# Optimization experiments

Hardware: AMD Instinct MI355X
Metric: run time of the kernel (lower is better)

Reference implementation:

```python
import jax, jax.numpy as jnp
import numpy as np

B, N, C = 8, 4096, 768
H = 12
D = C // H            # 64
BN = C // 2           # bottleneck dim 384
EPS_LN = 1e-5
EPS_ATTN = 1e-6


def layer_norm(x, g, b):
    mu = jnp.mean(x, axis=-1, keepdims=True)
    var = jnp.mean(jnp.square(x - mu), axis=-1, keepdims=True)
    return (x - mu) * jax.lax.rsqrt(var + EPS_LN) * g + b


def setup_inputs() -> dict:
    key = jax.random.key(0)
    ks = jax.random.split(key, 8)
    s = 0.02
    return {
        "x": jax.random.normal(ks[0], (B, N, C), jnp.float32),
        "w_qkv": jax.random.normal(ks[1], (C, 3 * C), jnp.float32) * s,
        "b_qkv": jnp.zeros((3 * C,), jnp.float32),
        "w_proj": jax.random.normal(ks[2], (C, C), jnp.float32) * s,
        "b_proj": jnp.zeros((C,), jnp.float32),
        "g1": jnp.ones((C,), jnp.float32),
        "beta1": jnp.zeros((C,), jnp.float32),
        "g2": jnp.ones((C,), jnp.float32),
        "beta2": jnp.zeros((C,), jnp.float32),
        "w_down": jax.random.normal(ks[3], (C, BN), jnp.float32) * s,
        "b_down": jnp.zeros((BN,), jnp.float32),
        "w_up": jax.random.normal(ks[4], (BN, C), jnp.float32) * s,
        "b_up": jnp.zeros((C,), jnp.float32),
        "g3": jnp.ones((C,), jnp.float32),
        "beta3": jnp.zeros((C,), jnp.float32),
    }


def _linear_attention(x, w_qkv, b_qkv, w_proj, b_proj):
    # x: (B, N, C)
    qkv = x @ w_qkv + b_qkv                       # (B, N, 3C)
    qkv = qkv.reshape(B, N, 3, H, D)
    qkv = jnp.transpose(qkv, (2, 0, 3, 1, 4))     # (3, B, H, N, D)
    q, k, v = qkv[0], qkv[1], qkv[2]
    fm = lambda t: jax.nn.elu(t) + 1.0            # positive feature map
    q, k = fm(q), fm(k)
    kv = jnp.einsum('bhnd,bhnv->bhdv', k, v)      # (B, H, D, D)
    out = jnp.einsum('bhnd,bhdv->bhnv', q, kv)    # (B, H, N, D)
    k_sum = k.sum(axis=2)                         # (B, H, D)
    normalizer = jnp.einsum('bhnd,bhd->bhn', q, k_sum) + EPS_ATTN
    out = out / normalizer[..., None]
    out = jnp.transpose(out, (0, 2, 1, 3)).reshape(B, N, C)
    return out @ w_proj + b_proj


def reference(x, w_qkv, b_qkv, w_proj, b_proj, g1, beta1, g2, beta2,
              w_down, b_down, w_up, b_up, g3, beta3):
    # DinomalyBlock forward (eval mode: dropout/noise disabled)
    x = x + _linear_attention(layer_norm(x, g1, beta1), w_qkv, b_qkv, w_proj, b_proj)
    r = layer_norm(x, g2, beta2)
    h = jax.nn.gelu(r @ w_down + b_down, approximate=False)  # torch GELU default = exact
    h = h @ w_up + b_up
    return layer_norm(r + h, g3, beta3)
```

## Files before the change

kernel.cpp:

```cpp
#include <hip/hip_runtime.h>
#include <hip/hip_bf16.h>
#include <cstdio>


typedef __attribute__((ext_vector_type(8))) short short8;
typedef __attribute__((ext_vector_type(4))) float floatx4;

__device__ __forceinline__ float bf2f(unsigned short u) {
    return __uint_as_float(((unsigned int)u) << 16);
}
__device__ __forceinline__ unsigned short f2bf(float f) {
    __hip_bfloat16 h = __float2bfloat16(f);
    return *reinterpret_cast<unsigned short*>(&h);
}

__device__ __forceinline__ void async_copy16(const unsigned short* g, unsigned short* l) {
    __builtin_amdgcn_global_load_lds(
        (const __attribute__((address_space(1))) unsigned int*)g,
        (__attribute__((address_space(3))) unsigned int*)l, 16, 0, 0);
}

__device__ __forceinline__ floatx4 MFMA16(short8 a, short8 b, floatx4 c) {
    return __builtin_amdgcn_mfma_f32_16x16x32_bf16(a, b, c, 0, 0, 0);
}

__global__ __launch_bounds__(256) void transpose_all(
    const float* __restrict__ wq, const float* __restrict__ wp,
    const float* __restrict__ wd, const float* __restrict__ wu,
    unsigned short* __restrict__ tq, unsigned short* __restrict__ tp,
    unsigned short* __restrict__ td, unsigned short* __restrict__ tu)
{
    int blk = blockIdx.x;
    const float* w; unsigned short* o; int K, Nc, tx32;
    if (blk < 1728)      { w = wq; o = tq; K = 768; Nc = 2304; tx32 = 24; }
    else if (blk < 2304) { w = wp; o = tp; K = 768; Nc = 768;  tx32 = 24; blk -= 1728; }
    else if (blk < 2592) { w = wd; o = td; K = 768; Nc = 384;  tx32 = 24; blk -= 2304; }
    else                 { w = wu; o = tu; K = 384; Nc = 768;  tx32 = 12; blk -= 2592; }
    int kb = (blk % tx32) * 32, nb = (blk / tx32) * 32;
    __shared__ float tile[32][33];
    int tx = threadIdx.x & 31, ty = threadIdx.x >> 5;
    #pragma unroll
    for (int i = 0; i < 32; i += 8)
        tile[ty + i][tx] = w[(size_t)(kb + ty + i) * Nc + nb + tx];
    __syncthreads();
    #pragma unroll
    for (int i = 0; i < 32; i += 8)
        o[(size_t)(nb + ty + i) * K + kb + tx] = f2bf(tile[tx][ty + i]);
}

template<bool OBF16>
__global__ __launch_bounds__(256) void ln_kernel(
    const float* __restrict__ in, const float* __restrict__ gw,
    const float* __restrict__ bw, void* __restrict__ outp)
{
    int t = threadIdx.x;
    int lane = t & 63, wave = t >> 6;
    int row = blockIdx.x * 4 + wave;
    const float4* src = (const float4*)(in + (size_t)row * 768);
    float4 x0 = src[lane], x1 = src[lane + 64], x2 = src[lane + 128];
    float s  = (x0.x + x0.y + x0.z + x0.w)
             + (x1.x + x1.y + x1.z + x1.w)
             + (x2.x + x2.y + x2.z + x2.w);
    float ss = (x0.x * x0.x + x0.y * x0.y + x0.z * x0.z + x0.w * x0.w)
             + (x1.x * x1.x + x1.y * x1.y + x1.z * x1.z + x1.w * x1.w)
             + (x2.x * x2.x + x2.y * x2.y + x2.z * x2.z + x2.w * x2.w);
    #pragma unroll
    for (int o = 1; o < 64; o <<= 1) {
        s += __shfl_xor(s, o);
        ss += __shfl_xor(ss, o);
    }
    float mu = s * (1.0f / 768.0f);
    float var = ss * (1.0f / 768.0f) - mu * mu;
    float rstd = rsqrtf(var + 1e-5f);
    float4 g0 = ((const float4*)gw)[lane], g1 = ((const float4*)gw)[lane + 64],
           g2 = ((const float4*)gw)[lane + 128];
    float4 b0 = ((const float4*)bw)[lane], b1 = ((const float4*)bw)[lane + 64],
           b2 = ((const float4*)bw)[lane + 128];
    float4 y0, y1, y2;
    y0.x = (x0.x - mu) * rstd * g0.x + b0.x; y0.y = (x0.y - mu) * rstd * g0.y + b0.y;
    y0.z = (x0.z - mu) * rstd * g0.z + b0.z; y0.w = (x0.w - mu) * rstd * g0.w + b0.w;
    y1.x = (x1.x - mu) * rstd * g1.x + b1.x; y1.y = (x1.y - mu) * rstd * g1.y + b1.y;
    y1.z = (x1.z - mu) * rstd * g1.z + b1.z; y1.w = (x1.w - mu) * rstd * g1.w + b1.w;
    y2.x = (x2.x - mu) * rstd * g2.x + b2.x; y2.y = (x2.y - mu) * rstd * g2.y + b2.y;
    y2.z = (x2.z - mu) * rstd * g2.z + b2.z; y2.w = (x2.w - mu) * rstd * g2.w + b2.w;
    if (OBF16) {
        uint2* dst = (uint2*)outp + (size_t)row * 192;
        uint2 p0, p1, p2;
        p0.x = (unsigned int)f2bf(y0.x) | ((unsigned int)f2bf(y0.y) << 16);
        p0.y = (unsigned int)f2bf(y0.z) | ((unsigned int)f2bf(y0.w) << 16);
        p1.x = (unsigned int)f2bf(y1.x) | ((unsigned int)f2bf(y1.y) << 16);
        p1.y = (unsigned int)f2bf(y1.z) | ((unsigned int)f2bf(y1.w) << 16);
        p2.x = (unsigned int)f2bf(y2.x) | ((unsigned int)f2bf(y2.y) << 16);
        p2.y = (unsigned int)f2bf(y2.z) | ((unsigned int)f2bf(y2.w) << 16);
        dst[lane] = p0; dst[lane + 64] = p1; dst[lane + 128] = p2;
    } else {
        float4* dst = (float4*)outp + (size_t)row * 192;
        dst[lane] = y0; dst[lane + 64] = y1; dst[lane + 128] = y2;
    }
}

template<bool RES_F32, bool OUT_F32>
__global__ __launch_bounds__(256) void add_ln_kernel(
    const unsigned short* __restrict__ y, const void* __restrict__ resv,
    const float* __restrict__ gw, const float* __restrict__ bw,
    void* __restrict__ outp)
{
    int t = threadIdx.x;
    int lane = t & 63, wave = t >> 6;
    int row = blockIdx.x * 4 + wave;
    const uint2* ysrc = (const uint2*)(y + (size_t)row * 768);
    uint2 ya = ysrc[lane], yb = ysrc[lane + 64], yc = ysrc[lane + 128];
    float v[12];
    v[0] = bf2f((unsigned short)(ya.x & 0xffff)); v[1] = bf2f((unsigned short)(ya.x >> 16));
    v[2] = bf2f((unsigned short)(ya.y & 0xffff)); v[3] = bf2f((unsigned short)(ya.y >> 16));
    v[4] = bf2f((unsigned short)(yb.x & 0xffff)); v[5] = bf2f((unsigned short)(yb.x >> 16));
    v[6] = bf2f((unsigned short)(yb.y & 0xffff)); v[7] = bf2f((unsigned short)(yb.y >> 16));
    v[8] = bf2f((unsigned short)(yc.x & 0xffff)); v[9] = bf2f((unsigned short)(yc.x >> 16));
    v[10] = bf2f((unsigned short)(yc.y & 0xffff)); v[11] = bf2f((unsigned short)(yc.y >> 16));
    if (RES_F32) {
        const float4* rsrc = (const float4*)((const float*)resv + (size_t)row * 768);
        float4 r0 = rsrc[lane], r1 = rsrc[lane + 64], r2 = rsrc[lane + 128];
        v[0] += r0.x; v[1] += r0.y; v[2] += r0.z; v[3] += r0.w;
        v[4] += r1.x; v[5] += r1.y; v[6] += r1.z; v[7] += r1.w;
        v[8] += r2.x; v[9] += r2.y; v[10] += r2.z; v[11] += r2.w;
    } else {
        const uint2* rsrc = (const uint2*)((const unsigned short*)resv + (size_t)row * 768);
        uint2 r0 = rsrc[lane], r1 = rsrc[lane + 64], r2 = rsrc[lane + 128];
        v[0] += bf2f((unsigned short)(r0.x & 0xffff)); v[1] += bf2f((unsigned short)(r0.x >> 16));
        v[2] += bf2f((unsigned short)(r0.y & 0xffff)); v[3] += bf2f((unsigned short)(r0.y >> 16));
        v[4] += bf2f((unsigned short)(r1.x & 0xffff)); v[5] += bf2f((unsigned short)(r1.x >> 16));
        v[6] += bf2f((unsigned short)(r1.y & 0xffff)); v[7] += bf2f((unsigned short)(r1.y >> 16));
        v[8] += bf2f((unsigned short)(r2.x & 0xffff)); v[9] += bf2f((unsigned short)(r2.x >> 16));
        v[10] += bf2f((unsigned short)(r2.y & 0xffff)); v[11] += bf2f((unsigned short)(r2.y >> 16));
    }
    float s = 0.f, ss = 0.f;
    #pragma unroll
    for (int i = 0; i < 12; i++) { s += v[i]; ss += v[i] * v[i]; }
    #pragma unroll
    for (int o = 1; o < 64; o <<= 1) {
        s += __shfl_xor(s, o);
        ss += __shfl_xor(ss, o);
    }
    float mu = s * (1.0f / 768.0f);
    float var = ss * (1.0f / 768.0f) - mu * mu;
    float rstd = rsqrtf(var + 1e-5f);
    float4 g0 = ((const float4*)gw)[lane], g1 = ((const float4*)gw)[lane + 64],
           g2 = ((const float4*)gw)[lane + 128];
    float4 b0 = ((const float4*)bw)[lane], b1 = ((const float4*)bw)[lane + 64],
           b2 = ((const float4*)bw)[lane + 128];
    float yv[12];
    yv[0] = (v[0] - mu) * rstd * g0.x + b0.x; yv[1] = (v[1] - mu) * rstd * g0.y + b0.y;
    yv[2] = (v[2] - mu) * rstd * g0.z + b0.z; yv[3] = (v[3] - mu) * rstd * g0.w + b0.w;
    yv[4] = (v[4] - mu) * rstd * g1.x + b1.x; yv[5] = (v[5] - mu) * rstd * g1.y + b1.y;
    yv[6] = (v[6] - mu) * rstd * g1.z + b1.z; yv[7] = (v[7] - mu) * rstd * g1.w + b1.w;
    yv[8] = (v[8] - mu) * rstd * g2.x + b2.x; yv[9] = (v[9] - mu) * rstd * g2.y + b2.y;
    yv[10] = (v[10] - mu) * rstd * g2.z + b2.z; yv[11] = (v[11] - mu) * rstd * g2.w + b2.w;
    if (OUT_F32) {
        float4* dst = (float4*)outp + (size_t)row * 192;
        dst[lane] = make_float4(yv[0], yv[1], yv[2], yv[3]);
        dst[lane + 64] = make_float4(yv[4], yv[5], yv[6], yv[7]);
        dst[lane + 128] = make_float4(yv[8], yv[9], yv[10], yv[11]);
    } else {
        uint2* dst = (uint2*)outp + (size_t)row * 192;
        uint2 p0, p1, p2;
        p0.x = (unsigned int)f2bf(yv[0]) | ((unsigned int)f2bf(yv[1]) << 16);
        p0.y = (unsigned int)f2bf(yv[2]) | ((unsigned int)f2bf(yv[3]) << 16);
        p1.x = (unsigned int)f2bf(yv[4]) | ((unsigned int)f2bf(yv[5]) << 16);
        p1.y = (unsigned int)f2bf(yv[6]) | ((unsigned int)f2bf(yv[7]) << 16);
        p2.x = (unsigned int)f2bf(yv[8]) | ((unsigned int)f2bf(yv[9]) << 16);
        p2.y = (unsigned int)f2bf(yv[10]) | ((unsigned int)f2bf(yv[11]) << 16);
        dst[lane] = p0; dst[lane + 64] = p1; dst[lane + 128] = p2;
    }
}

template<int MODE>
__global__ __launch_bounds__(256, 4) void gemm_kernel(
    const unsigned short* __restrict__ A,
    const unsigned short* __restrict__ Wt,
    const float* __restrict__ bias,
    unsigned short* __restrict__ outp,
    int M, int K, int Nc)
{
    __shared__ __align__(16) unsigned short As[128][64];
    __shared__ __align__(16) unsigned short Bs[128][64];
    const int row0 = blockIdx.y * 128;
    const int col0 = blockIdx.x * 128;
    const int t = threadIdx.x;
    const int lane = t & 63;
    const int wave = t >> 6;
    const int wm = (wave >> 1) * 64;
    const int wn = (wave & 1) * 64;
    const int frow = lane & 15;
    const int quad = lane >> 4;
    const int lrow = lane >> 3;
    const int lchunk = (lane & 7) ^ lrow;

    floatx4 acc[4][4];
    #pragma unroll
    for (int i = 0; i < 4; i++)
        #pragma unroll
        for (int j = 0; j < 4; j++)
            acc[i][j] = (floatx4){0.f, 0.f, 0.f, 0.f};

    for (int k0 = 0; k0 < K; k0 += 64) {
        __syncthreads();
        #pragma unroll
        for (int q = 0; q < 4; q++) {
            int r = wave * 32 + q * 8 + lrow;
            async_copy16(A  + (size_t)(row0 + r) * K + k0 + lchunk * 8, &As[wave * 32 + q * 8][0]);
            async_copy16(Wt + (size_t)(col0 + r) * K + k0 + lchunk * 8, &Bs[wave * 32 + q * 8][0]);
        }
        __syncthreads();
        #pragma unroll
        for (int ks = 0; ks < 2; ks++) {
            const int pc = ((ks * 4 + quad) ^ (frow & 7)) * 8;
            short8 af[4], bf4[4];
            #pragma unroll
            for (int i = 0; i < 4; i++) af[i] = *(const short8*)&As[wm + i * 16 + frow][pc];
            #pragma unroll
            for (int j = 0; j < 4; j++) bf4[j] = *(const short8*)&Bs[wn + j * 16 + frow][pc];
            #pragma unroll
            for (int i = 0; i < 4; i++)
                #pragma unroll
                for (int j = 0; j < 4; j++)
                    acc[i][j] = MFMA16(af[i], bf4[j], acc[i][j]);
        }
    }

    #pragma unroll
    for (int i = 0; i < 4; i++) {
        #pragma unroll
        for (int j = 0; j < 4; j++) {
            int col = col0 + wn + j * 16 + frow;
            float bcol = bias[col];
            #pragma unroll
            for (int rr = 0; rr < 4; rr++) {
                int row = row0 + wm + i * 16 + quad * 4 + rr;
                float v = acc[i][j][rr] + bcol;
                if (MODE == 0) {
                    if (col < 1536) v = (v > 0.f) ? (v + 1.f) : expf(v);
                } else if (MODE == 2) {
                    v = 0.5f * v * (1.0f + erff(v * 0.70710678118654752f));
                }
                outp[(size_t)row * Nc + col] = f2bf(v);
            }
        }
    }
}

__global__ __launch_bounds__(256, 4) void kv_accum(
    const unsigned short* __restrict__ qkv, float* __restrict__ kvbuf)
{
    int blk = blockIdx.x;
    int chunk = blk & 7;
    int bh = blk >> 3;
    int b = bh / 12, h = bh % 12;
    int n0 = chunk * 512;
    int t = threadIdx.x;
    int d = t & 63, g = t >> 6;
    __shared__ float kl[32][68];
    __shared__ float vl[32][68];
    float kv[16];
    #pragma unroll
    for (int j = 0; j < 16; j++) kv[j] = 0.f;
    float ks = 0.f;

    int sr = t >> 3;
    int c16 = (t & 7) * 16;
    bool isk = c16 < 64;
    int cc = isk ? c16 : c16 - 64;
    const unsigned short* gbase =
        qkv + (size_t)(b * 4096 + n0 + sr) * 2304 + (isk ? 768 : 1536) + h * 64 + cc;
    uint4 r0, r1;
    auto loadg = [&](int nb) {
        const uint4* s = (const uint4*)(gbase + (size_t)nb * 2304);
        r0 = s[0]; r1 = s[1];
    };
    auto storel = [&]() {
        float* dst = isk ? &kl[sr][cc] : &vl[sr][cc];
        const unsigned short* u0 = (const unsigned short*)&r0;
        const unsigned short* u1 = (const unsigned short*)&r1;
        #pragma unroll
        for (int i = 0; i < 8; i++) dst[i] = bf2f(u0[i]);
        #pragma unroll
        for (int i = 0; i < 8; i++) dst[8 + i] = bf2f(u1[i]);
    };

    loadg(0);
    for (int c = 0; c < 16; c++) {
        storel();
        __syncthreads();
        if (c < 15) loadg((c + 1) * 32);
        #pragma unroll 8
        for (int r2 = 0; r2 < 32; r2++) {
            float kd = kl[r2][d];
            ks += kd;
            const float4* vv = (const float4*)&vl[r2][g * 16];
            float4 a0 = vv[0], a1 = vv[1], a2 = vv[2], a3 = vv[3];
            kv[0]  += kd * a0.x; kv[1]  += kd * a0.y; kv[2]  += kd * a0.z; kv[3]  += kd * a0.w;
            kv[4]  += kd * a1.x; kv[5]  += kd * a1.y; kv[6]  += kd * a1.z; kv[7]  += kd * a1.w;
            kv[8]  += kd * a2.x; kv[9]  += kd * a2.y; kv[10] += kd * a2.z; kv[11] += kd * a2.w;
            kv[12] += kd * a3.x; kv[13] += kd * a3.y; kv[14] += kd * a3.z; kv[15] += kd * a3.w;
        }
        __syncthreads();
    }
    float* dstg = kvbuf + (size_t)bh * 4160;
    #pragma unroll
    for (int j = 0; j < 16; j++)
        atomicAdd(&dstg[(g * 16 + j) * 64 + d], kv[j]);
    if (g == 0) atomicAdd(&dstg[4096 + d], ks);
}

__global__ __launch_bounds__(256) void attn_apply(
    const unsigned short* __restrict__ qkv, const float* __restrict__ kvbuf,
    unsigned short* __restrict__ attnC)
{
    int blk = blockIdx.x;
    int nchunk = blk & 31;
    int bh = blk >> 5;
    int b = bh / 12, h = bh % 12;
    int n0 = nchunk * 128;
    int t = threadIdx.x;
    int lane = t & 63, wave = t >> 6;
    __shared__ __align__(16) unsigned short ql[128][72];
    __shared__ __align__(16) unsigned short Bs[80][72];

    {
        const float* kvg = kvbuf + (size_t)bh * 4160;
        int e = t >> 2, d0 = (t & 3) * 16;
        const float4* src4 = (const float4*)(kvg + e * 64 + d0);
        #pragma unroll
        for (int i = 0; i < 4; i++) {
            float4 v = src4[i];
            unsigned long long pk = (unsigned long long)f2bf(v.x)
                | ((unsigned long long)f2bf(v.y) << 16)
                | ((unsigned long long)f2bf(v.z) << 32)
                | ((unsigned long long)f2bf(v.w) << 48);
            *(unsigned long long*)&Bs[e][d0 + i * 4] = pk;
        }
        if (t < 64) {
            Bs[64][t] = f2bf(kvg[4096 + t]);
            #pragma unroll
            for (int r = 65; r < 80; r++) Bs[r][t] = 0;
        }
    }
    {
        int r = t >> 1, c0 = (t & 1) * 32;
        const uint4* src = (const uint4*)(qkv + (size_t)(b * 4096 + n0 + r) * 2304 + h * 64 + c0);
        uint4* dst = (uint4*)&ql[r][c0];
        #pragma unroll
        for (int i = 0; i < 4; i++) dst[i] = src[i];
    }
    __syncthreads();

    int frow = lane & 15, quad = lane >> 4;
    floatx4 acc[2][5];
    #pragma unroll
    for (int it = 0; it < 2; it++)
        #pragma unroll
        for (int jt = 0; jt < 5; jt++)
            acc[it][jt] = (floatx4){0.f, 0.f, 0.f, 0.f};

    #pragma unroll
    for (int ks = 0; ks < 2; ks++) {
        int fk = ks * 32 + quad * 8;
        short8 a0 = *(const short8*)&ql[wave * 32 + frow][fk];
        short8 a1 = *(const short8*)&ql[wave * 32 + 16 + frow][fk];
        #pragma unroll
        for (int jt = 0; jt < 5; jt++) {
            short8 bb = *(const short8*)&Bs[jt * 16 + frow][fk];
            acc[0][jt] = __builtin_amdgcn_mfma_f32_16x16x32_bf16(a0, bb, acc[0][jt], 0, 0, 0);
            acc[1][jt] = __builtin_amdgcn_mfma_f32_16x16x32_bf16(a1, bb, acc[1][jt], 0, 0, 0);
        }
    }

    #pragma unroll
    for (int it = 0; it < 2; it++) {
        #pragma unroll
        for (int rr = 0; rr < 4; rr++) {
            float nv = __shfl(acc[it][4][rr], (lane & 48));
            float inv = 1.0f / (nv + 1e-6f);
            int lr = it * 16 + quad * 4 + rr;
            #pragma unroll
            for (int jt = 0; jt < 4; jt++)
                ql[wave * 32 + lr][jt * 16 + frow] = f2bf(acc[it][jt][rr] * inv);
        }
    }
    #pragma unroll
    for (int j = 0; j < 4; j++) {
        int u = j * 64 + lane;
        int lr = u >> 3;
        int c8 = (u & 7) * 8;
        uint4 val = *(const uint4*)&ql[wave * 32 + lr][c8];
        int row = n0 + wave * 32 + lr;
        *(uint4*)&attnC[(size_t)(b * 4096 + row) * 768 + h * 64 + c8] = val;
    }
}

extern "C" void kernel_launch(void* const* d_in, const int* in_sizes, int n_in,
                              void* d_out, int out_size, void* d_ws, size_t ws_size,
                              hipStream_t stream)
{
    const float* x      = (const float*)d_in[0];
    const float* w_qkv  = (const float*)d_in[1];
    const float* b_qkv  = (const float*)d_in[2];
    const float* w_proj = (const float*)d_in[3];
    const float* b_proj = (const float*)d_in[4];
    const float* g1     = (const float*)d_in[5];
    const float* be1    = (const float*)d_in[6];
    const float* g2     = (const float*)d_in[7];
    const float* be2    = (const float*)d_in[8];
    const float* w_down = (const float*)d_in[9];
    const float* b_down = (const float*)d_in[10];
    const float* w_up   = (const float*)d_in[11];
    const float* b_up   = (const float*)d_in[12];
    const float* g3     = (const float*)d_in[13];
    const float* be3    = (const float*)d_in[14];

    char* p = (char*)d_ws;
    auto take = [&](size_t b) { char* q = p; p += (b + 255) & ~(size_t)255; return q; };
    unsigned short* wtq  = (unsigned short*)take((size_t)2304 * 768 * 2);
    unsigned short* wtp  = (unsigned short*)take((size_t)768 * 768 * 2);
    unsigned short* wtd  = (unsigned short*)take((size_t)384 * 768 * 2);
    unsigned short* wtu  = (unsigned short*)take((size_t)768 * 384 * 2);
    unsigned short* bufA = (unsigned short*)take((size_t)32768 * 768 * 2);
    unsigned short* qkvb = (unsigned short*)take((size_t)32768 * 2304 * 2);
    float*          kvb  = (float*)take((size_t)96 * 4160 * 4);
    unsigned short* hbuf = (unsigned short*)take((size_t)32768 * 384 * 2);
    unsigned short* rbuf    = qkvb;
    unsigned short* projout = qkvb + (size_t)32768 * 768;
    unsigned short* upout   = qkvb + (size_t)2 * 32768 * 768;

    size_t needed = (size_t)(p - (char*)d_ws);
    if (needed > ws_size)
        fprintf(stderr, "WARNING: ws too small: need %zu have %zu\n", needed, ws_size);

    transpose_all<<<2880, 256, 0, stream>>>(w_qkv, w_proj, w_down, w_up, wtq, wtp, wtd, wtu);
    hipMemsetAsync(kvb, 0, (size_t)96 * 4160 * 4, stream);

    ln_kernel<true><<<8192, 256, 0, stream>>>(x, g1, be1, bufA);
    gemm_kernel<0><<<dim3(18, 256), 256, 0, stream>>>(bufA, wtq, b_qkv, qkvb, 32768, 768, 2304);
    kv_accum<<<768, 256, 0, stream>>>(qkvb, kvb);
    attn_apply<<<3072, 256, 0, stream>>>(qkvb, kvb, bufA);
    gemm_kernel<1><<<dim3(6, 256), 256, 0, stream>>>(bufA, wtp, b_proj, projout, 32768, 768, 768);
    add_ln_kernel<true, false><<<8192, 256, 0, stream>>>(projout, x, g2, be2, rbuf);
    gemm_kernel<2><<<dim3(3, 256), 256, 0, stream>>>(rbuf, wtd, b_down, hbuf, 32768, 768, 384);
    gemm_kernel<1><<<dim3(6, 256), 256, 0, stream>>>(hbuf, wtu, b_up, upout, 32768, 384, 768);
    add_ln_kernel<false, true><<<8192, 256, 0, stream>>>(upout, rbuf, g3, be3, (float*)d_out);
}
```

Measured before the change: 611.9 us.

## Stage GEMM epilogue through LDS, merge prep kernels, widen add-LN loads

```diff
diff --git a/kernel.cpp b/kernel.cpp
--- a/kernel.cpp
+++ b/kernel.cpp
@@ -24,67 +24,74 @@
     return __builtin_amdgcn_mfma_f32_16x16x32_bf16(a, b, c, 0, 0, 0);
 }
 
-__global__ __launch_bounds__(256) void transpose_all(
+__device__ __forceinline__ void unpack8(uint4 c, float* v) {
+    v[0] = bf2f((unsigned short)(c.x & 0xffff)); v[1] = bf2f((unsigned short)(c.x >> 16));
+    v[2] = bf2f((unsigned short)(c.y & 0xffff)); v[3] = bf2f((unsigned short)(c.y >> 16));
+    v[4] = bf2f((unsigned short)(c.z & 0xffff)); v[5] = bf2f((unsigned short)(c.z >> 16));
+    v[6] = bf2f((unsigned short)(c.w & 0xffff)); v[7] = bf2f((unsigned short)(c.w >> 16));
+}
+
+__global__ __launch_bounds__(256) void prep_kernel(
     const float* __restrict__ wq, const float* __restrict__ wp,
     const float* __restrict__ wd, const float* __restrict__ wu,
     unsigned short* __restrict__ tq, unsigned short* __restrict__ tp,
-    unsigned short* __restrict__ td, unsigned short* __restrict__ tu)
+    unsigned short* __restrict__ td, unsigned short* __restrict__ tu,
+    const float* __restrict__ x, const float* __restrict__ g1,
+    const float* __restrict__ be1, unsigned short* __restrict__ ln1out,
+    float* __restrict__ kvb)
 {
     int blk = blockIdx.x;
-    const float* w; unsigned short* o; int K, Nc, tx32;
-    if (blk < 1728)      { w = wq; o = tq; K = 768; Nc = 2304; tx32 = 24; }
-    else if (blk < 2304) { w = wp; o = tp; K = 768; Nc = 768;  tx32 = 24; blk -= 1728; }
-    else if (blk < 2592) { w = wd; o = td; K = 768; Nc = 384;  tx32 = 24; blk -= 2304; }
-    else                 { w = wu; o = tu; K = 384; Nc = 768;  tx32 = 12; blk -= 2592; }
-    int kb = (blk % tx32) * 32, nb = (blk / tx32) * 32;
-    __shared__ float tile[32][33];
-    int tx = threadIdx.x & 31, ty = threadIdx.x >> 5;
-    #pragma unroll
-    for (int i = 0; i < 32; i += 8)
-        tile[ty + i][tx] = w[(size_t)(kb + ty + i) * Nc + nb + tx];
-    __syncthreads();
-    #pragma unroll
-    for (int i = 0; i < 32; i += 8)
-        o[(size_t)(nb + ty + i) * K + kb + tx] = f2bf(tile[tx][ty + i]);
-}
-
-template<bool OBF16>
-__global__ __launch_bounds__(256) void ln_kernel(
-    const float* __restrict__ in, const float* __restrict__ gw,
-    const float* __restrict__ bw, void* __restrict__ outp)
-{
-    int t = threadIdx.x;
-    int lane = t & 63, wave = t >> 6;
-    int row = blockIdx.x * 4 + wave;
-    const float4* src = (const float4*)(in + (size_t)row * 768);
-    float4 x0 = src[lane], x1 = src[lane + 64], x2 = src[lane + 128];
-    float s  = (x0.x + x0.y + x0.z + x0.w)
-             + (x1.x + x1.y + x1.z + x1.w)
-             + (x2.x + x2.y + x2.z + x2.w);
-    float ss = (x0.x * x0.x + x0.y * x0.y + x0.z * x0.z + x0.w * x0.w)
-             + (x1.x * x1.x + x1.y * x1.y + x1.z * x1.z + x1.w * x1.w)
-             + (x2.x * x2.x + x2.y * x2.y + x2.z * x2.z + x2.w * x2.w);
-    #pragma unroll
-    for (int o = 1; o < 64; o <<= 1) {
-        s += __shfl_xor(s, o);
-        ss += __shfl_xor(ss, o);
-    }
-    float mu = s * (1.0f / 768.0f);
-    float var = ss * (1.0f / 768.0f) - mu * mu;
-    float rstd = rsqrtf(var + 1e-5f);
-    float4 g0 = ((const float4*)gw)[lane], g1 = ((const float4*)gw)[lane + 64],
-           g2 = ((const float4*)gw)[lane + 128];
-    float4 b0 = ((const float4*)bw)[lane], b1 = ((const float4*)bw)[lane + 64],
-           b2 = ((const float4*)bw)[lane + 128];
-    float4 y0, y1, y2;
-    y0.x = (x0.x - mu) * rstd * g0.x + b0.x; y0.y = (x0.y - mu) * rstd * g0.y + b0.y;
-    y0.z = (x0.z - mu) * rstd * g0.z + b0.z; y0.w = (x0.w - mu) * rstd * g0.w + b0.w;
-    y1.x = (x1.x - mu) * rstd * g1.x + b1.x; y1.y = (x1.y - mu) * rstd * g1.y + b1.y;
-    y1.z = (x1.z - mu) * rstd * g1.z + b1.z; y1.w = (x1.w - mu) * rstd * g1.w + b1.w;
-    y2.x = (x2.x - mu) * rstd * g2.x + b2.x; y2.y = (x2.y - mu) * rstd * g2.y + b2.y;
-    y2.z = (x2.z - mu) * rstd * g2.z + b2.z; y2.w = (x2.w - mu) * rstd * g2.w + b2.w;
-    if (OBF16) {
-        uint2* dst = (uint2*)outp + (size_t)row * 192;
+    if (blk < 2880) {
+        const float* w; unsigned short* o; int K, Nc, tx32;
+        if (blk < 1728)      { w = wq; o = tq; K = 768; Nc = 2304; tx32 = 24; }
+        else if (blk < 2304) { w = wp; o = tp; K = 768; Nc = 768;  tx32 = 24; blk -= 1728; }
+        else if (blk < 2592) { w = wd; o = td; K = 768; Nc = 384;  tx32 = 24; blk -= 2304; }
+        else                 { w = wu; o = tu; K = 384; Nc = 768;  tx32 = 12; blk -= 2592; }
+        int kb = (blk % tx32) * 32, nb = (blk / tx32) * 32;
+        __shared__ float tile[32][33];
+        int tx = threadIdx.x & 31, ty = threadIdx.x >> 5;
+        #pragma unroll
+        for (int i = 0; i < 32; i += 8)
+            tile[ty + i][tx] = w[(size_t)(kb + ty + i) * Nc + nb + tx];
+        __syncthreads();
+        #pragma unroll
+        for (int i = 0; i < 32; i += 8)
+            o[(size_t)(nb + ty + i) * K + kb + tx] = f2bf(tile[tx][ty + i]);
+        return;
+    }
+    blk -= 2880;
+    if (blk < 8192) {
+        int t = threadIdx.x;
+        int lane = t & 63, wave = t >> 6;
+        int row = blk * 4 + wave;
+        const float4* src = (const float4*)(x + (size_t)row * 768);
+        float4 x0 = src[lane], x1 = src[lane + 64], x2 = src[lane + 128];
+        float s  = (x0.x + x0.y + x0.z + x0.w)
+                 + (x1.x + x1.y + x1.z + x1.w)
+                 + (x2.x + x2.y + x2.z + x2.w);
+        float ss = (x0.x * x0.x + x0.y * x0.y + x0.z * x0.z + x0.w * x0.w)
+                 + (x1.x * x1.x + x1.y * x1.y + x1.z * x1.z + x1.w * x1.w)
+                 + (x2.x * x2.x + x2.y * x2.y + x2.z * x2.z + x2.w * x2.w);
+        #pragma unroll
+        for (int o = 1; o < 64; o <<= 1) {
+            s += __shfl_xor(s, o);
+            ss += __shfl_xor(ss, o);
+        }
+        float mu = s * (1.0f / 768.0f);
+        float var = ss * (1.0f / 768.0f) - mu * mu;
+        float rstd = rsqrtf(var + 1e-5f);
+        float4 g0 = ((const float4*)g1)[lane], gg1 = ((const float4*)g1)[lane + 64],
+               g2 = ((const float4*)g1)[lane + 128];
+        float4 b0 = ((const float4*)be1)[lane], b1 = ((const float4*)be1)[lane + 64],
+               b2 = ((const float4*)be1)[lane + 128];
+        float4 y0, y1, y2;
+        y0.x = (x0.x - mu) * rstd * g0.x + b0.x; y0.y = (x0.y - mu) * rstd * g0.y + b0.y;
+        y0.z = (x0.z - mu) * rstd * g0.z + b0.z; y0.w = (x0.w - mu) * rstd * g0.w + b0.w;
+        y1.x = (x1.x - mu) * rstd * gg1.x + b1.x; y1.y = (x1.y - mu) * rstd * gg1.y + b1.y;
+        y1.z = (x1.z - mu) * rstd * gg1.z + b1.z; y1.w = (x1.w - mu) * rstd * gg1.w + b1.w;
+        y2.x = (x2.x - mu) * rstd * g2.x + b2.x; y2.y = (x2.y - mu) * rstd * g2.y + b2.y;
+        y2.z = (x2.z - mu) * rstd * g2.z + b2.z; y2.w = (x2.w - mu) * rstd * g2.w + b2.w;
+        uint2* dst = (uint2*)ln1out + (size_t)row * 192;
         uint2 p0, p1, p2;
         p0.x = (unsigned int)f2bf(y0.x) | ((unsigned int)f2bf(y0.y) << 16);
         p0.y = (unsigned int)f2bf(y0.z) | ((unsigned int)f2bf(y0.w) << 16);
@@ -93,10 +100,11 @@
         p2.x = (unsigned int)f2bf(y2.x) | ((unsigned int)f2bf(y2.y) << 16);
         p2.y = (unsigned int)f2bf(y2.z) | ((unsigned int)f2bf(y2.w) << 16);
         dst[lane] = p0; dst[lane + 64] = p1; dst[lane + 128] = p2;
-    } else {
-        float4* dst = (float4*)outp + (size_t)row * 192;
-        dst[lane] = y0; dst[lane + 64] = y1; dst[lane + 128] = y2;
-    }
+        return;
+    }
+    blk -= 8192;
+    int idx = blk * 256 + threadIdx.x;
+    ((float4*)kvb)[idx] = make_float4(0.f, 0.f, 0.f, 0.f);
 }
 
 template<bool RES_F32, bool OUT_F32>
@@ -106,70 +114,81 @@
     void* __restrict__ outp)
 {
     int t = threadIdx.x;
-    int lane = t & 63, wave = t >> 6;
-    int row = blockIdx.x * 4 + wave;
-    const uint2* ysrc = (const uint2*)(y + (size_t)row * 768);
-    uint2 ya = ysrc[lane], yb = ysrc[lane + 64], yc = ysrc[lane + 128];
-    float v[12];
-    v[0] = bf2f((unsigned short)(ya.x & 0xffff)); v[1] = bf2f((unsigned short)(ya.x >> 16));
-    v[2] = bf2f((unsigned short)(ya.y & 0xffff)); v[3] = bf2f((unsigned short)(ya.y >> 16));
-    v[4] = bf2f((unsigned short)(yb.x & 0xffff)); v[5] = bf2f((unsigned short)(yb.x >> 16));
-    v[6] = bf2f((unsigned short)(yb.y & 0xffff)); v[7] = bf2f((unsigned short)(yb.y >> 16));
-    v[8] = bf2f((unsigned short)(yc.x & 0xffff)); v[9] = bf2f((unsigned short)(yc.x >> 16));
-    v[10] = bf2f((unsigned short)(yc.y & 0xffff)); v[11] = bf2f((unsigned short)(yc.y >> 16));
+    int wave = t >> 6, lane = t & 63;
+    int half = lane >> 5, l = lane & 31;
+    int row = blockIdx.x * 8 + wave * 2 + half;
+    const uint4* ys = (const uint4*)(y + (size_t)row * 768);
+    uint4 c0 = ys[l], c1 = ys[l + 32], c2 = ys[l + 64];
+    float v[24];
+    unpack8(c0, v); unpack8(c1, v + 8); unpack8(c2, v + 16);
     if (RES_F32) {
-        const float4* rsrc = (const float4*)((const float*)resv + (size_t)row * 768);
-        float4 r0 = rsrc[lane], r1 = rsrc[lane + 64], r2 = rsrc[lane + 128];
-        v[0] += r0.x; v[1] += r0.y; v[2] += r0.z; v[3] += r0.w;
-        v[4] += r1.x; v[5] += r1.y; v[6] += r1.z; v[7] += r1.w;
-        v[8] += r2.x; v[9] += r2.y; v[10] += r2.z; v[11] += r2.w;
+        const float4* rs = (const float4*)((const float*)resv + (size_t)row * 768);
+        float4 r;
+        r = rs[2 * l];       v[0] += r.x;  v[1] += r.y;  v[2] += r.z;  v[3] += r.w;
+        r = rs[2 * l + 1];   v[4] += r.x;  v[5] += r.y;  v[6] += r.z;  v[7] += r.w;
+        r = rs[2 * l + 64];  v[8] += r.x;  v[9] += r.y;  v[10] += r.z; v[11] += r.w;
+        r = rs[2 * l + 65];  v[12] += r.x; v[13] += r.y; v[14] += r.z; v[15] += r.w;
+        r = rs[2 * l + 128]; v[16] += r.x; v[17] += r.y; v[18] += r.z; v[19] += r.w;
+        r = rs[2 * l + 129]; v[20] += r.x; v[21] += r.y; v[22] += r.z; v[23] += r.w;
     } else {
-        const uint2* rsrc = (const uint2*)((const unsigned short*)resv + (size_t)row * 768);
-        uint2 r0 = rsrc[lane], r1 = rsrc[lane + 64], r2 = rsrc[lane + 128];
-        v[0] += bf2f((unsigned short)(r0.x & 0xffff)); v[1] += bf2f((unsigned short)(r0.x >> 16));
-        v[2] += bf2f((unsigned short)(r0.y & 0xffff)); v[3] += bf2f((unsigned short)(r0.y >> 16));
-        v[4] += bf2f((unsigned short)(r1.x & 0xffff)); v[5] += bf2f((unsigned short)(r1.x >> 16));
-        v[6] += bf2f((unsigned short)(r1.y & 0xffff)); v[7] += bf2f((unsigned short)(r1.y >> 16));
-        v[8] += bf2f((unsigned short)(r2.x & 0xffff)); v[9] += bf2f((unsigned short)(r2.x >> 16));
-        v[10] += bf2f((unsigned short)(r2.y & 0xffff)); v[11] += bf2f((unsigned short)(r2.y >> 16));
+        const uint4* rs = (const uint4*)((const unsigned short*)resv + (size_t)row * 768);
+        uint4 d0 = rs[l], d1 = rs[l + 32], d2 = rs[l + 64];
+        float w[24];
+        unpack8(d0, w); unpack8(d1, w + 8); unpack8(d2, w + 16);
+        #pragma unroll
+        for (int i = 0; i < 24; i++) v[i] += w[i];
     }
     float s = 0.f, ss = 0.f;
     #pragma unroll
-    for (int i = 0; i < 12; i++) { s += v[i]; ss += v[i] * v[i]; }
-    #pragma unroll
-    for (int o = 1; o < 64; o <<= 1) {
+    for (int i = 0; i < 24; i++) { s += v[i]; ss += v[i] * v[i]; }
+    #pragma unroll
+    for (int o = 1; o < 32; o <<= 1) {
         s += __shfl_xor(s, o);
         ss += __shfl_xor(ss, o);
     }
     float mu = s * (1.0f / 768.0f);
     float var = ss * (1.0f / 768.0f) - mu * mu;
     float rstd = rsqrtf(var + 1e-5f);
-    float4 g0 = ((const float4*)gw)[lane], g1 = ((const float4*)gw)[lane + 64],
-           g2 = ((const float4*)gw)[lane + 128];
-    float4 b0 = ((const float4*)bw)[lane], b1 = ((const float4*)bw)[lane + 64],
-           b2 = ((const float4*)bw)[lane + 128];
-    float yv[12];
-    yv[0] = (v[0] - mu) * rstd * g0.x + b0.x; yv[1] = (v[1] - mu) * rstd * g0.y + b0.y;
-    yv[2] = (v[2] - mu) * rstd * g0.z + b0.z; yv[3] = (v[3] - mu) * rstd * g0.w + b0.w;
-    yv[4] = (v[4] - mu) * rstd * g1.x + b1.x; yv[5] = (v[5] - mu) * rstd * g1.y + b1.y;
-    yv[6] = (v[6] - mu) * rstd * g1.z + b1.z; yv[7] = (v[7] - mu) * rstd * g1.w + b1.w;
-    yv[8] = (v[8] - mu) * rstd * g2.x + b2.x; yv[9] = (v[9] - mu) * rstd * g2.y + b2.y;
-    yv[10] = (v[10] - mu) * rstd * g2.z + b2.z; yv[11] = (v[11] - mu) * rstd * g2.w + b2.w;
+    float yv[24];
+    {
+        const float4* gp = (const float4*)gw;
+        const float4* bp = (const float4*)bw;
+        int gi[6] = {2 * l, 2 * l + 1, 2 * l + 64, 2 * l + 65, 2 * l + 128, 2 * l + 129};
+        #pragma unroll
+        for (int q = 0; q < 6; q++) {
+            float4 g = gp[gi[q]], b = bp[gi[q]];
+            yv[q * 4 + 0] = (v[q * 4 + 0] - mu) * rstd * g.x + b.x;
+            yv[q * 4 + 1] = (v[q * 4 + 1] - mu) * rstd * g.y + b.y;
+            yv[q * 4 + 2] = (v[q * 4 + 2] - mu) * rstd * g.z + b.z;
+            yv[q * 4 + 3] = (v[q * 4 + 3] - mu) * rstd * g.w + b.w;
+        }
+    }
     if (OUT_F32) {
         float4* dst = (float4*)outp + (size_t)row * 192;
-        dst[lane] = make_float4(yv[0], yv[1], yv[2], yv[3]);
-        dst[lane + 64] = make_float4(yv[4], yv[5], yv[6], yv[7]);
-        dst[lane + 128] = make_float4(yv[8], yv[9], yv[10], yv[11]);
+        dst[2 * l]       = make_float4(yv[0], yv[1], yv[2], yv[3]);
+        dst[2 * l + 1]   = make_float4(yv[4], yv[5], yv[6], yv[7]);
+        dst[2 * l + 64]  = make_float4(yv[8], yv[9], yv[10], yv[11]);
+        dst[2 * l + 65]  = make_float4(yv[12], yv[13], yv[14], yv[15]);
+        dst[2 * l + 128] = make_float4(yv[16], yv[17], yv[18], yv[19]);
+        dst[2 * l + 129] = make_float4(yv[20], yv[21], yv[22], yv[23]);
     } else {
-        uint2* dst = (uint2*)outp + (size_t)row * 192;
-        uint2 p0, p1, p2;
-        p0.x = (unsigned int)f2bf(yv[0]) | ((unsigned int)f2bf(yv[1]) << 16);
-        p0.y = (unsigned int)f2bf(yv[2]) | ((unsigned int)f2bf(yv[3]) << 16);
-        p1.x = (unsigned int)f2bf(yv[4]) | ((unsigned int)f2bf(yv[5]) << 16);
-        p1.y = (unsigned int)f2bf(yv[6]) | ((unsigned int)f2bf(yv[7]) << 16);
-        p2.x = (unsigned int)f2bf(yv[8]) | ((unsigned int)f2bf(yv[9]) << 16);
-        p2.y = (unsigned int)f2bf(yv[10]) | ((unsigned int)f2bf(yv[11]) << 16);
-        dst[lane] = p0; dst[lane + 64] = p1; dst[lane + 128] = p2;
+        uint4* dst = (uint4*)outp + (size_t)row * 96;
+        uint4 p;
+        p.x = (unsigned int)f2bf(yv[0]) | ((unsigned int)f2bf(yv[1]) << 16);
+        p.y = (unsigned int)f2bf(yv[2]) | ((unsigned int)f2bf(yv[3]) << 16);
+        p.z = (unsigned int)f2bf(yv[4]) | ((unsigned int)f2bf(yv[5]) << 16);
+        p.w = (unsigned int)f2bf(yv[6]) | ((unsigned int)f2bf(yv[7]) << 16);
+        dst[l] = p;
+        p.x = (unsigned int)f2bf(yv[8])  | ((unsigned int)f2bf(yv[9]) << 16);
+        p.y = (unsigned int)f2bf(yv[10]) | ((unsigned int)f2bf(yv[11]) << 16);
+        p.z = (unsigned int)f2bf(yv[12]) | ((unsigned int)f2bf(yv[13]) << 16);
+        p.w = (unsigned int)f2bf(yv[14]) | ((unsigned int)f2bf(yv[15]) << 16);
+        dst[l + 32] = p;
+        p.x = (unsigned int)f2bf(yv[16]) | ((unsigned int)f2bf(yv[17]) << 16);
+        p.y = (unsigned int)f2bf(yv[18]) | ((unsigned int)f2bf(yv[19]) << 16);
+        p.z = (unsigned int)f2bf(yv[20]) | ((unsigned int)f2bf(yv[21]) << 16);
+        p.w = (unsigned int)f2bf(yv[22]) | ((unsigned int)f2bf(yv[23]) << 16);
+        dst[l + 64] = p;
     }
 }
 
@@ -227,6 +246,8 @@
         }
     }
 
+    __syncthreads();
+    unsigned short* cstage = (wave < 2 ? &As[0][0] : &Bs[0][0]) + (wave & 1) * 4096;
     #pragma unroll
     for (int i = 0; i < 4; i++) {
         #pragma unroll
@@ -235,16 +256,27 @@
             float bcol = bias[col];
             #pragma unroll
             for (int rr = 0; rr < 4; rr++) {
-                int row = row0 + wm + i * 16 + quad * 4 + rr;
                 float v = acc[i][j][rr] + bcol;
                 if (MODE == 0) {
                     if (col < 1536) v = (v > 0.f) ? (v + 1.f) : expf(v);
                 } else if (MODE == 2) {
                     v = 0.5f * v * (1.0f + erff(v * 0.70710678118654752f));
                 }
-                outp[(size_t)row * Nc + col] = f2bf(v);
+                int lr = i * 16 + quad * 4 + rr;
+                int c  = j * 16 + frow;
+                int swz = (c >> 3) ^ (lr & 7);
+                cstage[lr * 64 + swz * 8 + (c & 7)] = f2bf(v);
             }
         }
+    }
+    #pragma unroll
+    for (int it = 0; it < 8; it++) {
+        int u = it * 64 + lane;
+        int r = u >> 3;
+        int ch = u & 7;
+        int swz = ch ^ (r & 7);
+        uint4 val = *(const uint4*)&cstage[r * 64 + swz * 8];
+        *(uint4*)&outp[(size_t)(row0 + wm + r) * Nc + col0 + wn + ch * 8] = val;
     }
 }
 
@@ -435,16 +467,15 @@
     if (needed > ws_size)
         fprintf(stderr, "WARNING: ws too small: need %zu have %zu\n", needed, ws_size);
 
-    transpose_all<<<2880, 256, 0, stream>>>(w_qkv, w_proj, w_down, w_up, wtq, wtp, wtd, wtu);
-    hipMemsetAsync(kvb, 0, (size_t)96 * 4160 * 4, stream);
-
-    ln_kernel<true><<<8192, 256, 0, stream>>>(x, g1, be1, bufA);
+    prep_kernel<<<11462, 256, 0, stream>>>(w_qkv, w_proj, w_down, w_up,
+                                           wtq, wtp, wtd, wtu,
+                                           x, g1, be1, bufA, kvb);
     gemm_kernel<0><<<dim3(18, 256), 256, 0, stream>>>(bufA, wtq, b_qkv, qkvb, 32768, 768, 2304);
     kv_accum<<<768, 256, 0, stream>>>(qkvb, kvb);
     attn_apply<<<3072, 256, 0, stream>>>(qkvb, kvb, bufA);
     gemm_kernel<1><<<dim3(6, 256), 256, 0, stream>>>(bufA, wtp, b_proj, projout, 32768, 768, 768);
-    add_ln_kernel<true, false><<<8192, 256, 0, stream>>>(projout, x, g2, be2, rbuf);
+    add_ln_kernel<true, false><<<4096, 256, 0, stream>>>(projout, x, g2, be2, rbuf);
     gemm_kernel<2><<<dim3(3, 256), 256, 0, stream>>>(rbuf, wtd, b_down, hbuf, 32768, 768, 384);
     gemm_kernel<1><<<dim3(6, 256), 256, 0, stream>>>(hbuf, wtu, b_up, upout, 32768, 384, 768);
-    add_ln_kernel<false, true><<<8192, 256, 0, stream>>>(upout, rbuf, g3, be3, (float*)d_out);
-}
+    add_ln_kernel<false, true><<<4096, 256, 0, stream>>>(upout, rbuf, g3, be3, (float*)d_out);
+}
```

New measurement: 652.1 us. +6.6%, slower.
